# Performance work log

Hardware: AMD Instinct MI355X
Metric: run time of the kernel (lower is better)

## Reference

```python
import jax, jax.numpy as jnp
import numpy as np

T, B, LAG, H = 128, 1024, 6, 256


def setup_inputs() -> dict:
    key = jax.random.key(0)
    ks = jax.random.split(key, 16)
    s = 0.05  # small init scale to keep LSTM gates in a sane range
    d = {}
    d["x"] = jax.random.normal(ks[0], (T, B, LAG), jnp.float32)
    d["Wi1"] = jax.random.normal(ks[1], (H, LAG), jnp.float32) * s
    d["bi1"] = jnp.zeros((H,), jnp.float32)
    d["Wi2"] = jax.random.normal(ks[2], (H, H), jnp.float32) * s
    d["bi2"] = jnp.zeros((H,), jnp.float32)
    d["Wi3"] = jax.random.normal(ks[3], (H, H), jnp.float32) * s
    d["bi3"] = jnp.zeros((H,), jnp.float32)
    d["Wih0"] = jax.random.normal(ks[4], (4 * H, H), jnp.float32) * s
    d["Whh0"] = jax.random.normal(ks[5], (4 * H, H), jnp.float32) * s
    d["bih0"] = jnp.zeros((4 * H,), jnp.float32)
    d["bhh0"] = jnp.zeros((4 * H,), jnp.float32)
    d["Wih1"] = jax.random.normal(ks[6], (4 * H, H), jnp.float32) * s
    d["Whh1"] = jax.random.normal(ks[7], (4 * H, H), jnp.float32) * s
    d["bih1"] = jnp.zeros((4 * H,), jnp.float32)
    d["bhh1"] = jnp.zeros((4 * H,), jnp.float32)
    d["Wo1"] = jax.random.normal(ks[8], (H, H), jnp.float32) * s
    d["bo1"] = jnp.zeros((H,), jnp.float32)
    d["Wo2"] = jax.random.normal(ks[9], (H, H), jnp.float32) * s
    d["bo2"] = jnp.zeros((H,), jnp.float32)
    d["Wo3"] = jax.random.normal(ks[10], (LAG, H), jnp.float32) * s
    d["bo3"] = jnp.zeros((LAG,), jnp.float32)
    return d


def _lstm_cell(xt, h, c, Wih, Whh, bih, bhh):
    # PyTorch gate order: i, f, g, o
    g = xt @ Wih.T + h @ Whh.T + (bih + bhh)
    i, f, gg, o = jnp.split(g, 4, axis=-1)
    c2 = jax.nn.sigmoid(f) * c + jax.nn.sigmoid(i) * jnp.tanh(gg)
    h2 = jax.nn.sigmoid(o) * jnp.tanh(c2)
    return h2, c2


def reference(x, Wi1, bi1, Wi2, bi2, Wi3, bi3,
              Wih0, Whh0, bih0, bhh0, Wih1, Whh1, bih1, bhh1,
              Wo1, bo1, Wo2, bo2, Wo3, bo3):
    relu = jax.nn.relu
    # input MLP applied to every timestep at once: [T,B,6] -> [T,B,H]
    u = relu(x @ Wi1.T + bi1)
    u = relu(u @ Wi2.T + bi2)
    u = relu(u @ Wi3.T + bi3)

    def step(carry, xt):
        h0, c0, h1, c1 = carry
        h0, c0 = _lstm_cell(xt, h0, c0, Wih0, Whh0, bih0, bhh0)
        # dropout(0.05) between layers is identity in eval mode
        h1, c1 = _lstm_cell(h0, h1, c1, Wih1, Whh1, bih1, bhh1)
        return (h0, c0, h1, c1), h1

    z = jnp.zeros((x.shape[1], Whh0.shape[1]), x.dtype)
    _, hs = jax.lax.scan(step, (z, z, z, z), u)  # hs: [T,B,H]

    # output MLP: ReLU, Linear, ReLU, Linear, ReLU, Linear(H->6)
    y = relu(hs)
    y = relu(y @ Wo1.T + bo1)
    y = relu(y @ Wo2.T + bo2)
    y = y @ Wo3.T + bo3
    return y  # [T,B,6]
```

## Files before the change

### kernel.cpp

```cpp
#include <hip/hip_runtime.h>
#include <math.h>


namespace {
constexpr int kT   = 128;
constexpr int kB   = 1024;
constexpr int kLag = 6;
constexpr int kH   = 256;
constexpr int kTc  = 32;
constexpr int kMc  = kTc * kB;
constexpr int kGS  = 67;
constexpr int kLdsBytes = 2 * 32768 + 2 * 64 * kGS * 4;
}

typedef _Float16 half8 __attribute__((ext_vector_type(8)));
typedef _Float16 half2 __attribute__((ext_vector_type(2)));
typedef float f32x4 __attribute__((ext_vector_type(4)));
typedef unsigned long long u64;

__device__ __forceinline__ float sigm(float x) {
    return 1.f / (1.f + exp2f(-1.4426950408889634f * x));
}
__device__ __forceinline__ float tanh_(float x) {
    return 2.f / (1.f + exp2f(-2.8853900817779268f * x)) - 1.f;
}

__device__ __forceinline__ half8 pack(u64 a, u64 b) {
    union { u64 u[2]; half8 h; } r;
    r.u[0] = a; r.u[1] = b;
    return r.h;
}

__device__ __forceinline__ void ld_l2(half8& d, const _Float16* p) {
    asm volatile("global_load_dwordx4 %0, %1, off sc0"
                 : "=v"(d) : "v"(p) : "memory");
}
#define WAITCNT_HOLD8(A, B)                                                   \
    asm volatile("s_waitcnt vmcnt(0)"                                         \
        : "+v"(A[0]), "+v"(A[1]), "+v"(A[2]), "+v"(A[3]),                     \
          "+v"(B[0]), "+v"(B[1]), "+v"(B[2]), "+v"(B[3]))

__global__ __launch_bounds__(256)
void zero_fill(unsigned int* __restrict__ p)
{
    p[blockIdx.x * 256 + threadIdx.x] = 0u;
}

__global__ __launch_bounds__(256)
void cvt_f2h(const float* __restrict__ s, _Float16* __restrict__ d)
{
    const int i = blockIdx.x * 256 + threadIdx.x;
    d[i] = (_Float16)s[i];
}

__global__ __launch_bounds__(256)
void build_wcat(const float* __restrict__ Wih, const float* __restrict__ Whh,
                _Float16* __restrict__ d)
{
    const int i = blockIdx.x * 256 + threadIdx.x;
    const int row = i >> 9, col = i & 511;
    const float v = (col < 256) ? Wih[row * 256 + col] : Whh[row * 256 + col - 256];
    d[i] = (_Float16)v;
}

__global__ __launch_bounds__(256)
void add_bias(const float* __restrict__ a, const float* __restrict__ b,
              float* __restrict__ d)
{
    const int i = blockIdx.x * 256 + threadIdx.x;
    d[i] = a[i] + b[i];
}

__global__ __launch_bounds__(256)
void in_mlp1(const float* __restrict__ x, const float* __restrict__ Wi1,
             const float* __restrict__ bi1, _Float16* __restrict__ out)
{
    const int idx = blockIdx.x * 256 + threadIdx.x;
    const int col = idx & (kH - 1);
    const int row = idx >> 8;
    const float* xr = x + (size_t)row * kLag;
    const float* w  = Wi1 + col * kLag;
    float s = bi1[col];
#pragma unroll
    for (int k = 0; k < kLag; ++k) s = fmaf(xr[k], w[k], s);
    out[idx] = (_Float16)fmaxf(s, 0.f);
}

__global__ __launch_bounds__(256)
void gemm_h16(const _Float16* __restrict__ A, const _Float16* __restrict__ W,
              const float* __restrict__ bias, _Float16* __restrict__ C)
{
    const int tid = threadIdx.x;
    const int w = tid >> 6, lane = tid & 63, q = lane >> 4, l15 = lane & 15;
    const int n0 = blockIdx.x * 64;
    const int r0 = blockIdx.y * 128 + w * 32;

    half8 bf[4][8];
#pragma unroll
    for (int nt = 0; nt < 4; ++nt)
#pragma unroll
        for (int kk = 0; kk < 8; ++kk)
            bf[nt][kk] = *(const half8*)(W + (size_t)(n0 + nt * 16 + l15) * 256
                                         + kk * 32 + q * 8);
    float bz[4];
#pragma unroll
    for (int nt = 0; nt < 4; ++nt) bz[nt] = bias[n0 + nt * 16 + l15];

#pragma unroll
    for (int rt = 0; rt < 2; ++rt) {
        const _Float16* arow = A + (size_t)(r0 + rt * 16 + l15) * 256 + q * 8;
        half8 af[8];
#pragma unroll
        for (int kk = 0; kk < 8; ++kk) af[kk] = *(const half8*)(arow + kk * 32);
        f32x4 acc[4];
#pragma unroll
        for (int nt = 0; nt < 4; ++nt)
            acc[nt] = (f32x4){bz[nt], bz[nt], bz[nt], bz[nt]};
#pragma unroll
        for (int kk = 0; kk < 8; ++kk)
#pragma unroll
            for (int nt = 0; nt < 4; ++nt)
                acc[nt] = __builtin_amdgcn_mfma_f32_16x16x32_f16(
                    af[kk], bf[nt][kk], acc[nt], 0, 0, 0);
#pragma unroll
        for (int nt = 0; nt < 4; ++nt)
#pragma unroll
            for (int r = 0; r < 4; ++r) {
                const float v = fmaxf(acc[nt][r], 0.f);
                C[(size_t)(r0 + rt * 16 + q * 4 + r) * 256 + n0 + nt * 16 + l15]
                    = (_Float16)v;
            }
    }
}

__device__ __forceinline__ void waitpeers(const unsigned int* __restrict__ fb,
                                          unsigned int target, int tid)
{
    if (tid < 64) {
        const unsigned int* fp = fb + (tid & 15) * 16;
        unsigned int v;
        do {
            v = __hip_atomic_load(fp, __ATOMIC_RELAXED,
                                  __HIP_MEMORY_SCOPE_AGENT);
        } while (__any(v < target));
    }
    __syncthreads();
}

__device__ __forceinline__ void gather_lo(const _Float16* lo, int row, int q,
                                          u64* ua)
{
    const u64* plo = (const u64*)(lo + (size_t)row * 256 + q * 8);
#pragma unroll
    for (int kk = 0; kk < 8; ++kk) {
        ua[2*kk]   = plo[kk*8];
        ua[2*kk+1] = plo[kk*8 + 1];
    }
}

__device__ __forceinline__ void gstore(float* __restrict__ gl, int m0, int nb,
                                       int q, int l15,
                                       const f32x4& a0, const f32x4& a1)
{
#pragma unroll
    for (int r = 0; r < 4; ++r) {
        gl[(m0 + q*4 + r) * kGS + nb + l15]      = a0[r];
        gl[(m0 + q*4 + r) * kGS + nb + 16 + l15] = a1[r];
    }
}

__device__ __forceinline__ void phase_gemm_lds2(
    const char* pA, const char* pB,
    const half8 (&B0)[16], const half8 (&B1)[16],
    float* __restrict__ gl, int rtb, int nb, int q, int l15)
{
#pragma unroll
    for (int rt = 0; rt < 2; ++rt) {
        const int row = (rtb + rt) * 16 + l15;
        const int xr  = ((row & 15) << 4) ^ ((row & 1) << 8);
        const int rb  = row * 512;
        f32x4 a0 = {0.f,0.f,0.f,0.f}, a1 = {0.f,0.f,0.f,0.f};
#pragma unroll
        for (int kk = 0; kk < 8; ++kk) {
            const int off = rb + ((q * 16 + kk * 64) ^ xr);
            const half8 alo = *(const half8*)(pA + off);
            const half8 ahi = *(const half8*)(pB + off);
            a0 = __builtin_amdgcn_mfma_f32_16x16x32_f16(alo, B0[kk],     a0, 0,0,0);
            a1 = __builtin_amdgcn_mfma_f32_16x16x32_f16(alo, B1[kk],     a1, 0,0,0);
            a0 = __builtin_amdgcn_mfma_f32_16x16x32_f16(ahi, B0[8 + kk], a0, 0,0,0);
            a1 = __builtin_amdgcn_mfma_f32_16x16x32_f16(ahi, B1[8 + kk], a1, 0,0,0);
        }
        gstore(gl, (rtb + rt) * 16, nb, q, l15, a0, a1);
    }
}

__device__ __forceinline__ void phase_gemm_l0(
    const _Float16* __restrict__ u, const char* pH0,
    const half8 (&B0)[16], const half8 (&B1)[16],
    float* __restrict__ gl, int rtb, int nb, int q, int l15)
{
    half8 uf[2][8];
#pragma unroll
    for (int rt = 0; rt < 2; ++rt) {
        const _Float16* pu = u + (size_t)((rtb + rt) * 16 + l15) * 256 + q * 8;
#pragma unroll
        for (int kk = 0; kk < 8; ++kk)
            uf[rt][kk] = *(const half8*)(pu + kk * 32);
    }
#pragma unroll
    for (int rt = 0; rt < 2; ++rt) {
        const int row = (rtb + rt) * 16 + l15;
        const int xr  = ((row & 15) << 4) ^ ((row & 1) << 8);
        const int rb  = row * 512;
        f32x4 a0 = {0.f,0.f,0.f,0.f}, a1 = {0.f,0.f,0.f,0.f};
#pragma unroll
        for (int kk = 0; kk < 8; ++kk) {
            const int off = rb + ((q * 16 + kk * 64) ^ xr);
            const half8 ah = *(const half8*)(pH0 + off);
            a0 = __builtin_amdgcn_mfma_f32_16x16x32_f16(uf[rt][kk], B0[kk], a0, 0,0,0);
            a1 = __builtin_amdgcn_mfma_f32_16x16x32_f16(uf[rt][kk], B1[kk], a1, 0,0,0);
            a0 = __builtin_amdgcn_mfma_f32_16x16x32_f16(ah, B0[8 + kk],     a0, 0,0,0);
            a1 = __builtin_amdgcn_mfma_f32_16x16x32_f16(ah, B1[8 + kk],     a1, 0,0,0);
        }
        gstore(gl, (rtb + rt) * 16, nb, q, l15, a0, a1);
    }
}

__device__ __forceinline__ void cell_one(const float* __restrict__ gl,
    int crow, int cc, const float* __restrict__ bs, float* __restrict__ cst,
    _Float16* __restrict__ hout, _Float16* __restrict__ uout)
{
    const float* gr = gl + crow * kGS;
    _Float16 hp[2];
#pragma unroll
    for (int e = 0; e < 2; ++e) {
        const float gi = gr[0*16 + cc + e] + bs[e*4 + 0];
        const float gf = gr[1*16 + cc + e] + bs[e*4 + 1];
        const float gg = gr[2*16 + cc + e] + bs[e*4 + 2];
        const float go = gr[3*16 + cc + e] + bs[e*4 + 3];
        const float c2 = sigm(gf) * cst[e] + sigm(gi) * tanh_(gg);
        cst[e] = c2;
        hp[e] = (_Float16)(sigm(go) * tanh_(c2));
    }
    *(half2*)(hout + (size_t)crow * 256 + cc) = (half2){hp[0], hp[1]};
    if (uout) {
        const _Float16 z = (_Float16)0.f;
        *(half2*)(uout + (size_t)crow * 256 + cc) =
            (half2){hp[0] > z ? hp[0] : z, hp[1] > z ? hp[1] : z};
    }
}

__global__ __launch_bounds__(512, 2)
void lstm_all(_Float16* __restrict__ ubuf,
              const _Float16* __restrict__ Wc0, const _Float16* __restrict__ Wc1,
              const float* __restrict__ bc0, const float* __restrict__ bc1,
              _Float16* __restrict__ h0b, _Float16* __restrict__ h1b,
              unsigned int* __restrict__ cnt)
{
    extern __shared__ char lds[];
    char* pH0  = lds;
    char* pH1  = lds + 32768;
    float* gl0 = (float*)(lds + 65536);
    float* gl1 = gl0 + 64 * kGS;

    const int tid = threadIdx.x;
    const int w = tid >> 6, lane = tid & 63, q = lane >> 4, l15 = lane & 15;
    const int wl = w & 3;
    const int rtb = (wl >> 1) * 2;
    const int nb  = (wl & 1) * 32;
    const int lyr = (w < 4) ? 1 : 0;

    __shared__ int sh_bi, sh_js;
    if (tid == 0) {
        unsigned int xcd = __builtin_amdgcn_s_getreg(20 | (31 << 11)) & 7u;
        unsigned int rank = __hip_atomic_fetch_add(cnt + 4096 + xcd * 16, 1u,
            __ATOMIC_RELAXED, __HIP_MEMORY_SCOPE_AGENT);
        sh_bi = (int)(xcd * 2 + (rank >> 4));
        sh_js = (int)(rank & 15);
    }
    __syncthreads();
    const int bi = sh_bi, js = sh_js;
    unsigned int* fb    = cnt + (size_t)bi * 256;
    unsigned int* fslot = fb + js * 16;

    const _Float16* WcL = lyr ? Wc1 : Wc0;
    half8 Bf0[16], Bf1[16];
    {
        const _Float16* wr0 = WcL
            + (size_t)((nb >> 4) * 256 + js * 16 + l15) * 512 + q * 8;
        const _Float16* wr1 = WcL
            + (size_t)(((nb >> 4) + 1) * 256 + js * 16 + l15) * 512 + q * 8;
#pragma unroll
        for (int kk = 0; kk < 16; ++kk) {
            Bf0[kk] = *(const half8*)(wr0 + kk * 32);
            Bf1[kk] = *(const half8*)(wr1 + kk * 32);
        }
    }

    int sdst[4];
#pragma unroll
    for (int r = 0; r < 4; ++r) {
        const int L   = tid * 16 + r * 8192;
        const int row = L >> 9;
        const int c   = L & 511;
        sdst[r] = row * 512 + (c ^ ((row & 15) << 4) ^ ((row & 1) << 8));
    }

    const int cc = (tid & 7) * 2;
    const int crow = tid >> 3;
    float bs0[8], bs1[8];
#pragma unroll
    for (int e = 0; e < 2; ++e)
#pragma unroll
        for (int g = 0; g < 4; ++g) {
            bs0[e*4 + g] = bc0[g * 256 + js * 16 + cc + e];
            bs1[e*4 + g] = bc1[g * 256 + js * 16 + cc + e];
        }
    float cst0[2] = {0.f, 0.f}, cst1[2] = {0.f, 0.f};
    const size_t rbase = (size_t)bi * 64 * 256;
    const size_t obase = rbase + js * 16;

    if (lyr == 0) {
#pragma unroll
        for (int rt = 0; rt < 2; ++rt) {
            u64 ua[16];
            gather_lo(ubuf + rbase, (rtb + rt) * 16 + l15, q, ua);
            f32x4 a0 = {0.f,0.f,0.f,0.f}, a1 = {0.f,0.f,0.f,0.f};
#pragma unroll
            for (int kk = 0; kk < 8; ++kk) {
                const half8 af = pack(ua[2*kk], ua[2*kk+1]);
                a0 = __builtin_amdgcn_mfma_f32_16x16x32_f16(af, Bf0[kk], a0, 0,0,0);
                a1 = __builtin_amdgcn_mfma_f32_16x16x32_f16(af, Bf1[kk], a1, 0,0,0);
            }
            gstore(gl0, (rtb + rt) * 16, nb, q, l15, a0, a1);
        }
    }
    __syncthreads();
    cell_one(gl0, crow, cc, bs0, cst0, h0b + obase, nullptr);
    asm volatile("s_waitcnt vmcnt(0)" ::: "memory");
    __syncthreads();
    if (tid == 0)
        __hip_atomic_fetch_add(fslot, 1u, __ATOMIC_RELAXED,
                               __HIP_MEMORY_SCOPE_AGENT);

    for (int t = 0; t < kT; ++t) {
        const size_t p  = (size_t)(t & 1) * kB * 256;
        const size_t pn = (size_t)((t & 1) ^ 1) * kB * 256;
        const bool hasB = (t < kT - 1);

        waitpeers(fb, (unsigned)(t + 1), tid);

        {
            half8 s0[4], s1h[4];
            const char* b0 = (const char*)(h0b + p  + rbase);
            const char* b1 = (const char*)(h1b + pn + rbase);
#pragma unroll
            for (int r = 0; r < 4; ++r) {
                ld_l2(s0[r],  (const _Float16*)(b0 + tid * 16 + r * 8192));
                ld_l2(s1h[r], (const _Float16*)(b1 + tid * 16 + r * 8192));
            }
            WAITCNT_HOLD8(s0, s1h);
#pragma unroll
            for (int r = 0; r < 4; ++r) {
                *(half8*)(pH0 + sdst[r]) = s0[r];
                *(half8*)(pH1 + sdst[r]) = s1h[r];
            }
        }
        __syncthreads();

        if (lyr == 1) {
            phase_gemm_lds2(pH0, pH1, Bf0, Bf1, gl1, rtb, nb, q, l15);
        } else if (hasB) {
            phase_gemm_l0(ubuf + (size_t)(t + 1) * kB * 256 + rbase, pH0,
                          Bf0, Bf1, gl0, rtb, nb, q, l15);
        }
        __syncthreads();

        cell_one(gl1, crow, cc, bs1, cst1, h1b + p + obase,
                 ubuf + (size_t)t * kB * 256 + obase);
        if (hasB) {
            cell_one(gl0, crow, cc, bs0, cst0, h0b + pn + obase, nullptr);
            asm volatile("s_waitcnt vmcnt(0)" ::: "memory");
            __syncthreads();
            if (tid == 0)
                __hip_atomic_fetch_add(fslot, 1u, __ATOMIC_RELAXED,
                                       __HIP_MEMORY_SCOPE_AGENT);
        }
    }
}

__global__ __launch_bounds__(256)
void out_mlp3(const _Float16* __restrict__ y2, const float* __restrict__ Wo3,
              const float* __restrict__ bo3, float* __restrict__ out)
{
    const int lane = threadIdx.x & 63;
    const int row  = blockIdx.x * 4 + (threadIdx.x >> 6);
    const _Float16* yr = y2 + (size_t)row * kH + lane * 4;
    const float a0 = (float)yr[0], a1 = (float)yr[1], a2 = (float)yr[2], a3 = (float)yr[3];
    float s[kLag];
#pragma unroll
    for (int o = 0; o < kLag; ++o) {
        const float4 wv = *(const float4*)(Wo3 + o * kH + lane * 4);
        s[o] = a0 * wv.x + a1 * wv.y + a2 * wv.z + a3 * wv.w;
    }
#pragma unroll
    for (int off = 32; off > 0; off >>= 1) {
#pragma unroll
        for (int o = 0; o < kLag; ++o) s[o] += __shfl_down(s[o], off);
    }
    if (lane == 0) {
#pragma unroll
        for (int o = 0; o < kLag; ++o)
            out[(size_t)row * kLag + o] = s[o] + bo3[o];
    }
}

extern "C" void kernel_launch(void* const* d_in, const int* in_sizes, int n_in,
                              void* d_out, int out_size, void* d_ws, size_t ws_size,
                              hipStream_t stream)
{
    const float* x    = (const float*)d_in[0];
    const float* Wi1  = (const float*)d_in[1];
    const float* bi1  = (const float*)d_in[2];
    const float* Wi2  = (const float*)d_in[3];
    const float* bi2  = (const float*)d_in[4];
    const float* Wi3  = (const float*)d_in[5];
    const float* bi3  = (const float*)d_in[6];
    const float* Wih0 = (const float*)d_in[7];
    const float* Whh0 = (const float*)d_in[8];
    const float* bih0 = (const float*)d_in[9];
    const float* bhh0 = (const float*)d_in[10];
    const float* Wih1 = (const float*)d_in[11];
    const float* Whh1 = (const float*)d_in[12];
    const float* bih1 = (const float*)d_in[13];
    const float* bhh1 = (const float*)d_in[14];
    const float* Wo1  = (const float*)d_in[15];
    const float* bo1  = (const float*)d_in[16];
    const float* Wo2  = (const float*)d_in[17];
    const float* bo2  = (const float*)d_in[18];
    const float* Wo3  = (const float*)d_in[19];
    const float* bo3  = (const float*)d_in[20];
    float* outp = (float*)d_out;

    char* p = (char*)d_ws;
    _Float16* ubuf = (_Float16*)p;  p += (size_t)kT * kB * kH * 2;
    _Float16* s1   = (_Float16*)p;  p += (size_t)kMc * kH * 2;
    _Float16* s2   = (_Float16*)p;  p += (size_t)kMc * kH * 2;
    _Float16* Wc0  = (_Float16*)p;  p += (size_t)1024 * 512 * 2;
    _Float16* Wc1  = (_Float16*)p;  p += (size_t)1024 * 512 * 2;
    _Float16* W2h  = (_Float16*)p;  p += (size_t)kH * kH * 2;
    _Float16* W3h  = (_Float16*)p;  p += (size_t)kH * kH * 2;
    _Float16* Wo1h = (_Float16*)p;  p += (size_t)kH * kH * 2;
    _Float16* Wo2h = (_Float16*)p;  p += (size_t)kH * kH * 2;
    float* bc0 = (float*)p;  p += 1024 * 4;
    float* bc1 = (float*)p;  p += 1024 * 4;
    _Float16* h0b = (_Float16*)p;  p += (size_t)2 * kB * kH * 2;
    _Float16* h1b = (_Float16*)p;  p += (size_t)2 * kB * kH * 2;
    unsigned int* cnt = (unsigned int*)p;  p += 17408;

    zero_fill<<<2065, 256, 0, stream>>>((unsigned int*)h0b);
    cvt_f2h<<<kH * kH / 256, 256, 0, stream>>>(Wi2, W2h);
    cvt_f2h<<<kH * kH / 256, 256, 0, stream>>>(Wi3, W3h);
    cvt_f2h<<<kH * kH / 256, 256, 0, stream>>>(Wo1, Wo1h);
    cvt_f2h<<<kH * kH / 256, 256, 0, stream>>>(Wo2, Wo2h);
    build_wcat<<<1024 * 512 / 256, 256, 0, stream>>>(Wih0, Whh0, Wc0);
    build_wcat<<<1024 * 512 / 256, 256, 0, stream>>>(Wih1, Whh1, Wc1);
    add_bias<<<4, 256, 0, stream>>>(bih0, bhh0, bc0);
    add_bias<<<4, 256, 0, stream>>>(bih1, bhh1, bc1);

    for (int c = 0; c < kT / kTc; ++c) {
        in_mlp1<<<kMc * kH / 256, 256, 0, stream>>>(
            x + (size_t)c * kMc * kLag, Wi1, bi1, s1);
        gemm_h16<<<dim3(4, kMc / 128), 256, 0, stream>>>(s1, W2h, bi2, s2);
        gemm_h16<<<dim3(4, kMc / 128), 256, 0, stream>>>(
            s2, W3h, bi3, ubuf + (size_t)c * kMc * kH);
    }

    static bool attr_set = false;
    if (!attr_set) {
        hipFuncSetAttribute((const void*)lstm_all,
                            hipFuncAttributeMaxDynamicSharedMemorySize, kLdsBytes);
        attr_set = true;
    }
    void* args[] = {&ubuf, &Wc0, &Wc1, &bc0, &bc1, &h0b, &h1b, &cnt};
    hipLaunchCooperativeKernel((const void*)lstm_all, dim3(256), dim3(512),
                               args, kLdsBytes, stream);

    for (int c = 0; c < kT / kTc; ++c) {
        gemm_h16<<<dim3(4, kMc / 128), 256, 0, stream>>>(
            ubuf + (size_t)c * kMc * kH, Wo1h, bo1, s1);
        gemm_h16<<<dim3(4, kMc / 128), 256, 0, stream>>>(s1, Wo2h, bo2, s2);
        out_mlp3<<<kMc / 4, 256, 0, stream>>>(
            s2, Wo3, bo3, outp + (size_t)c * kMc * kLag);
    }
}
```

Before: 2.023 ms.

## Interleave LSTM gate weights so each wave applies cell update to its own tile

```diff
diff --git a/kernel.cpp b/kernel.cpp
--- a/kernel.cpp
+++ b/kernel.cpp
@@ -9,12 +9,14 @@
 constexpr int kH   = 256;
 constexpr int kTc  = 32;
 constexpr int kMc  = kTc * kB;
-constexpr int kGS  = 67;
+constexpr int kGS  = 68;
 constexpr int kLdsBytes = 2 * 32768 + 2 * 64 * kGS * 4;
+constexpr int kRankMain = 4096;
+constexpr int kCntUints = 16384;
 }
 
 typedef _Float16 half8 __attribute__((ext_vector_type(8)));
-typedef _Float16 half2 __attribute__((ext_vector_type(2)));
+typedef _Float16 half4 __attribute__((ext_vector_type(4)));
 typedef float f32x4 __attribute__((ext_vector_type(4)));
 typedef unsigned long long u64;
 
@@ -54,12 +56,16 @@
 }
 
 __global__ __launch_bounds__(256)
-void build_wcat(const float* __restrict__ Wih, const float* __restrict__ Whh,
-                _Float16* __restrict__ d)
+void build_wcat2(const float* __restrict__ Wih, const float* __restrict__ Whh,
+                 _Float16* __restrict__ d)
 {
     const int i = blockIdx.x * 256 + threadIdx.x;
     const int row = i >> 9, col = i & 511;
-    const float v = (col < 256) ? Wih[row * 256 + col] : Whh[row * 256 + col - 256];
+    const int js = row >> 6, r6 = row & 63;
+    const int tt = r6 >> 4, e = r6 & 15;
+    const int c = e >> 2, g = e & 3;
+    const int src = g * 256 + js * 16 + tt * 4 + c;
+    const float v = (col < 256) ? Wih[src * 256 + col] : Whh[src * 256 + col - 256];
     d[i] = (_Float16)v;
 }
 
@@ -226,27 +232,30 @@
     }
 }
 
-__device__ __forceinline__ void cell_one(const float* __restrict__ gl,
-    int crow, int cc, const float* __restrict__ bs, float* __restrict__ cst,
+__device__ __forceinline__ void cells_wave(const float* __restrict__ gl,
+    int grow, int hclb, const float* __restrict__ bs, float* __restrict__ cst,
     _Float16* __restrict__ hout, _Float16* __restrict__ uout)
 {
-    const float* gr = gl + crow * kGS;
-    _Float16 hp[2];
-#pragma unroll
-    for (int e = 0; e < 2; ++e) {
-        const float gi = gr[0*16 + cc + e] + bs[e*4 + 0];
-        const float gf = gr[1*16 + cc + e] + bs[e*4 + 1];
-        const float gg = gr[2*16 + cc + e] + bs[e*4 + 2];
-        const float go = gr[3*16 + cc + e] + bs[e*4 + 3];
-        const float c2 = sigm(gf) * cst[e] + sigm(gi) * tanh_(gg);
-        cst[e] = c2;
-        hp[e] = (_Float16)(sigm(go) * tanh_(c2));
-    }
-    *(half2*)(hout + (size_t)crow * 256 + cc) = (half2){hp[0], hp[1]};
+    const float* gr = gl + grow * kGS + hclb * 4;
+    half4 hv;
+#pragma unroll
+    for (int c = 0; c < 4; ++c) {
+        const f32x4 g4 = *(const f32x4*)(gr + c * 4);
+        const float gi = g4[0] + bs[c*4 + 0];
+        const float gf = g4[1] + bs[c*4 + 1];
+        const float gg = g4[2] + bs[c*4 + 2];
+        const float go = g4[3] + bs[c*4 + 3];
+        const float c2 = sigm(gf) * cst[c] + sigm(gi) * tanh_(gg);
+        cst[c] = c2;
+        hv[c] = (_Float16)(sigm(go) * tanh_(c2));
+    }
+    *(half4*)(hout + (size_t)grow * 256 + hclb) = hv;
     if (uout) {
         const _Float16 z = (_Float16)0.f;
-        *(half2*)(uout + (size_t)crow * 256 + cc) =
-            (half2){hp[0] > z ? hp[0] : z, hp[1] > z ? hp[1] : z};
+        half4 uv;
+#pragma unroll
+        for (int c = 0; c < 4; ++c) uv[c] = hv[c] > z ? hv[c] : z;
+        *(half4*)(uout + (size_t)grow * 256 + hclb) = uv;
     }
 }
 
@@ -267,13 +276,14 @@
     const int w = tid >> 6, lane = tid & 63, q = lane >> 4, l15 = lane & 15;
     const int wl = w & 3;
     const int rtb = (wl >> 1) * 2;
-    const int nb  = (wl & 1) * 32;
+    const int nbw = wl & 1;
+    const int nb  = nbw * 32;
     const int lyr = (w < 4) ? 1 : 0;
 
     __shared__ int sh_bi, sh_js;
     if (tid == 0) {
         unsigned int xcd = __builtin_amdgcn_s_getreg(20 | (31 << 11)) & 7u;
-        unsigned int rank = __hip_atomic_fetch_add(cnt + 4096 + xcd * 16, 1u,
+        unsigned int rank = __hip_atomic_fetch_add(cnt + kRankMain + xcd * 16, 1u,
             __ATOMIC_RELAXED, __HIP_MEMORY_SCOPE_AGENT);
         sh_bi = (int)(xcd * 2 + (rank >> 4));
         sh_js = (int)(rank & 15);
@@ -287,9 +297,9 @@
     half8 Bf0[16], Bf1[16];
     {
         const _Float16* wr0 = WcL
-            + (size_t)((nb >> 4) * 256 + js * 16 + l15) * 512 + q * 8;
+            + (size_t)(js * 64 + (nbw * 2    ) * 16 + l15) * 512 + q * 8;
         const _Float16* wr1 = WcL
-            + (size_t)(((nb >> 4) + 1) * 256 + js * 16 + l15) * 512 + q * 8;
+            + (size_t)(js * 64 + (nbw * 2 + 1) * 16 + l15) * 512 + q * 8;
 #pragma unroll
         for (int kk = 0; kk < 16; ++kk) {
             Bf0[kk] = *(const half8*)(wr0 + kk * 32);
@@ -306,19 +316,18 @@
         sdst[r] = row * 512 + (c ^ ((row & 15) << 4) ^ ((row & 1) << 8));
     }
 
-    const int cc = (tid & 7) * 2;
-    const int crow = tid >> 3;
-    float bs0[8], bs1[8];
-#pragma unroll
-    for (int e = 0; e < 2; ++e)
-#pragma unroll
-        for (int g = 0; g < 4; ++g) {
-            bs0[e*4 + g] = bc0[g * 256 + js * 16 + cc + e];
-            bs1[e*4 + g] = bc1[g * 256 + js * 16 + cc + e];
-        }
-    float cst0[2] = {0.f, 0.f}, cst1[2] = {0.f, 0.f};
+    const int grow = rtb * 16 + (lane >> 1);
+    const int hclb = nbw * 8 + (lane & 1) * 4;
+    const float* bcL = lyr ? bc1 : bc0;
+    float bs[16];
+#pragma unroll
+    for (int c = 0; c < 4; ++c)
+#pragma unroll
+        for (int g = 0; g < 4; ++g)
+            bs[c*4 + g] = bcL[g * 256 + js * 16 + hclb + c];
+    float cst[4] = {0.f, 0.f, 0.f, 0.f};
     const size_t rbase = (size_t)bi * 64 * 256;
-    const size_t obase = rbase + js * 16;
+    const size_t hoff  = rbase + js * 16;
 
     if (lyr == 0) {
 #pragma unroll
@@ -334,9 +343,8 @@
             }
             gstore(gl0, (rtb + rt) * 16, nb, q, l15, a0, a1);
         }
-    }
-    __syncthreads();
-    cell_one(gl0, crow, cc, bs0, cst0, h0b + obase, nullptr);
+        cells_wave(gl0, grow, hclb, bs, cst, (_Float16*)(h0b + hoff), nullptr);
+    }
     asm volatile("s_waitcnt vmcnt(0)" ::: "memory");
     __syncthreads();
     if (tid == 0)
@@ -370,22 +378,21 @@
 
         if (lyr == 1) {
             phase_gemm_lds2(pH0, pH1, Bf0, Bf1, gl1, rtb, nb, q, l15);
+            cells_wave(gl1, grow, hclb, bs, cst,
+                       (_Float16*)(h1b + p + hoff),
+                       (_Float16*)(ubuf + (size_t)t * kB * 256 + hoff));
         } else if (hasB) {
             phase_gemm_l0(ubuf + (size_t)(t + 1) * kB * 256 + rbase, pH0,
                           Bf0, Bf1, gl0, rtb, nb, q, l15);
+            cells_wave(gl0, grow, hclb, bs, cst,
+                       (_Float16*)(h0b + pn + hoff), nullptr);
         }
+
+        asm volatile("s_waitcnt vmcnt(0)" ::: "memory");
         __syncthreads();
-
-        cell_one(gl1, crow, cc, bs1, cst1, h1b + p + obase,
-                 ubuf + (size_t)t * kB * 256 + obase);
-        if (hasB) {
-            cell_one(gl0, crow, cc, bs0, cst0, h0b + pn + obase, nullptr);
-            asm volatile("s_waitcnt vmcnt(0)" ::: "memory");
-            __syncthreads();
-            if (tid == 0)
-                __hip_atomic_fetch_add(fslot, 1u, __ATOMIC_RELAXED,
-                                       __HIP_MEMORY_SCOPE_AGENT);
-        }
+        if (hasB && tid == 0)
+            __hip_atomic_fetch_add(fslot, 1u, __ATOMIC_RELAXED,
+                                   __HIP_MEMORY_SCOPE_AGENT);
     }
 }
 
@@ -456,15 +463,15 @@
     float* bc1 = (float*)p;  p += 1024 * 4;
     _Float16* h0b = (_Float16*)p;  p += (size_t)2 * kB * kH * 2;
     _Float16* h1b = (_Float16*)p;  p += (size_t)2 * kB * kH * 2;
-    unsigned int* cnt = (unsigned int*)p;  p += 17408;
-
-    zero_fill<<<2065, 256, 0, stream>>>((unsigned int*)h0b);
+    unsigned int* cnt = (unsigned int*)p;  p += kCntUints * 4;
+
+    zero_fill<<<2112, 256, 0, stream>>>((unsigned int*)h0b);
     cvt_f2h<<<kH * kH / 256, 256, 0, stream>>>(Wi2, W2h);
     cvt_f2h<<<kH * kH / 256, 256, 0, stream>>>(Wi3, W3h);
     cvt_f2h<<<kH * kH / 256, 256, 0, stream>>>(Wo1, Wo1h);
     cvt_f2h<<<kH * kH / 256, 256, 0, stream>>>(Wo2, Wo2h);
-    build_wcat<<<1024 * 512 / 256, 256, 0, stream>>>(Wih0, Whh0, Wc0);
-    build_wcat<<<1024 * 512 / 256, 256, 0, stream>>>(Wih1, Whh1, Wc1);
+    build_wcat2<<<1024 * 512 / 256, 256, 0, stream>>>(Wih0, Whh0, Wc0);
+    build_wcat2<<<1024 * 512 / 256, 256, 0, stream>>>(Wih1, Whh1, Wc1);
     add_bias<<<4, 256, 0, stream>>>(bih0, bhh0, bc0);
     add_bias<<<4, 256, 0, stream>>>(bih1, bhh1, bc1);
 
```

Result: no change. 2.031 ms (+0.4%).
